# Kernel optimization log

Measured on AMD Instinct MI355X. Metric: run time of the kernel, lower is better.

## Reference

```python
import jax, jax.numpy as jnp
import numpy as np

B, T, D = 8, 128, 512


def setup_inputs() -> dict:
    key = jax.random.key(0)
    ks = jax.random.split(key, 13)
    s = 1.0 / np.sqrt(D)
    inp = {"x": jax.random.normal(ks[0], (B, T, D), dtype=jnp.float32)}
    names = ["qf", "kf", "vf", "qt", "kt", "vt"]
    for i, n in enumerate(names):
        inp[f"W_{n}"] = jax.random.uniform(ks[1 + 2 * i], (D, D), dtype=jnp.float32, minval=-s, maxval=s)
        inp[f"b_{n}"] = jax.random.uniform(ks[2 + 2 * i], (D,), dtype=jnp.float32, minval=-s, maxval=s)
    return inp


def reference(x, W_qf, b_qf, W_kf, b_kf, W_vf, b_vf, W_qt, b_qt, W_kt, b_kt, W_vt, b_vt):
    # torch nn.Linear stores weight as [out, in]: y = x @ W.T + b
    lin = lambda h, W, b: jnp.einsum('bti,oi->bto', h, W) + b

    # --- feature branch: elementwise Q*K scores, softmax over feature dim ---
    Q_f = lin(x, W_qf, b_qf)
    K_f = lin(x, W_kf, b_kf)
    V_f = lin(x, W_vf, b_vf)
    ctx_f = jax.nn.softmax(Q_f * K_f, axis=-1) * V_f  # [B,T,D]

    # --- temporal(-named) branch: per-(b,t) outer product over feature dim ---
    Q_t = lin(x, W_qt, b_qt)
    K_t = lin(x, W_kt, b_kt)
    V_t = lin(x, W_vt, b_vt)
    scores_t = jnp.einsum('bti,btj->btij', Q_t, K_t)          # [B,T,D,D]
    probs_t = jax.nn.softmax(scores_t, axis=-1)
    ctx_t = jnp.einsum('btij,btj->bti', probs_t, V_t)          # [B,T,D]

    # dropout is identity in eval mode
    return ctx_f + ctx_t
```

## Files before the change

### kernel.cpp

```cpp
#include <hip/hip_runtime.h>
#include <hip/hip_bf16.h>
#include <math.h>


#define M_ROWS 1024
#define DIMD   512
#define NCOLS  3072
#define KPHYS  1024

typedef __attribute__((ext_vector_type(8))) short short8;
typedef __attribute__((ext_vector_type(4))) float f32x4;

struct PtrArgs {
    const float* W[6];
    const float* b[6];
};

#define XN (M_ROWS * DIMD)
#define WN (NCOLS * DIMD)

__device__ __forceinline__ unsigned short bf16_rne(float v) {
    unsigned u = __float_as_uint(v);
    u = (u + 0x7FFFu + ((u >> 16) & 1u)) >> 16;
    return (unsigned short)u;
}

__device__ __constant__ float INVFACT[25] = {
    1.0f, 1.0f, 0.5f,
    1.6666666666666666e-01f, 4.1666666666666664e-02f, 8.3333333333333332e-03f,
    1.3888888888888889e-03f, 1.9841269841269841e-04f, 2.4801587301587302e-05f,
    2.7557319223985893e-06f, 2.7557319223985888e-07f, 2.5052108385441720e-08f,
    2.0876756987868100e-09f, 1.6059043836821613e-10f, 1.1470745597729725e-11f,
    7.6471637318198164e-13f, 4.7794773323873853e-14f, 2.8114572543455206e-15f,
    1.5619206968586225e-16f, 8.2206352466243295e-18f, 4.1103176233121648e-19f,
    1.9572941063391263e-20f, 8.8967913924505741e-22f, 3.8681701706306835e-23f,
    1.6117375710961184e-24f
};

__global__ __launch_bounds__(256) void convert_split(const float* __restrict__ x,
                                                     PtrArgs pa,
                                                     unsigned short* __restrict__ Aph,
                                                     unsigned short* __restrict__ Bph,
                                                     float* __restrict__ biasAll) {
    int idx = blockIdx.x * 256 + threadIdx.x;
    if (idx < NCOLS) {
        biasAll[idx] = pa.b[idx >> 9][idx & 511];
    }
    if (idx < XN) {
        int m = idx >> 9, k = idx & 511;
        int s = k >> 5, p = k & 31;
        float v = x[idx];
        unsigned short hb = bf16_rne(v);
        float hf = __uint_as_float(((unsigned)hb) << 16);
        unsigned short lb = bf16_rne(v - hf);
        Aph[(size_t)m * KPHYS + s * 64 + p]      = hb;
        Aph[(size_t)m * KPHYS + s * 64 + 32 + p] = lb;
    } else if (idx < XN + WN) {
        int j = idx - XN;
        int n = j >> 9, k = j & 511;
        int g = n >> 9, o = n & 511;
        int s = k >> 5, p = k & 31;
        float v = pa.W[g][(size_t)o * DIMD + k];
        unsigned short hb = bf16_rne(v);
        float hf = __uint_as_float(((unsigned)hb) << 16);
        unsigned short lb = bf16_rne(v - hf);
        Bph[(size_t)n * KPHYS + s * 64 + p]      = hb;
        Bph[(size_t)n * KPHYS + s * 64 + 32 + p] = lb;
    }
}

__global__ __launch_bounds__(256) void gemm_mfma(const unsigned short* __restrict__ A,
                                                 const unsigned short* __restrict__ B,
                                                 const float* __restrict__ biasAll,
                                                 float* __restrict__ Y) {
    __shared__ __align__(16) short As[64 * 128];
    __shared__ __align__(16) short Bs[128 * 128];

    const int tid  = threadIdx.x;
    const int m0   = blockIdx.y * 64;
    const int n0   = blockIdx.x * 128;
    const int lane = tid & 63;
    const int w    = tid >> 6;
    const int wm   = w & 1;
    const int wn   = w >> 1;
    const int l15  = lane & 15;
    const int quad = lane >> 4;

    f32x4 acc[2][4];
    #pragma unroll
    for (int i = 0; i < 2; ++i)
        #pragma unroll
        for (int j = 0; j < 4; ++j)
            acc[i][j] = (f32x4){0.f, 0.f, 0.f, 0.f};

    for (int it = 0; it < 8; ++it) {
        const int kbase = it * 128;
        __syncthreads();
        #pragma unroll
        for (int t = 0; t < 4; ++t) {
            int idx = t * 256 + tid;
            int r = idx >> 4, c = idx & 15;
            int cc = c ^ (r & 15);
            const unsigned short* ga = A + (size_t)(m0 + r) * KPHYS + kbase + cc * 8;
            __builtin_amdgcn_global_load_lds(
                (const __attribute__((address_space(1))) unsigned int*)ga,
                (__attribute__((address_space(3))) unsigned int*)&As[idx * 8], 16, 0, 0);
        }
        #pragma unroll
        for (int t = 0; t < 8; ++t) {
            int idx = t * 256 + tid;
            int r = idx >> 4, c = idx & 15;
            int cc = c ^ (r & 15);
            const unsigned short* gb = B + (size_t)(n0 + r) * KPHYS + kbase + cc * 8;
            __builtin_amdgcn_global_load_lds(
                (const __attribute__((address_space(1))) unsigned int*)gb,
                (__attribute__((address_space(3))) unsigned int*)&Bs[idx * 8], 16, 0, 0);
        }
        __syncthreads();

        #pragma unroll
        for (int kk = 0; kk < 2; ++kk) {
            short8 ah[2], al[2], bh[4], bl[4];
            #pragma unroll
            for (int mt = 0; mt < 2; ++mt) {
                int rA = wm * 32 + mt * 16 + l15;
                int ch = (kk * 8 + quad)     ^ (rA & 15);
                int cl = (kk * 8 + 4 + quad) ^ (rA & 15);
                ah[mt] = *(const short8*)&As[(rA * 16 + ch) * 8];
                al[mt] = *(const short8*)&As[(rA * 16 + cl) * 8];
            }
            #pragma unroll
            for (int nt = 0; nt < 4; ++nt) {
                int rB = wn * 64 + nt * 16 + l15;
                int ch = (kk * 8 + quad)     ^ (rB & 15);
                int cl = (kk * 8 + 4 + quad) ^ (rB & 15);
                bh[nt] = *(const short8*)&Bs[(rB * 16 + ch) * 8];
                bl[nt] = *(const short8*)&Bs[(rB * 16 + cl) * 8];
            }
            #pragma unroll
            for (int mt = 0; mt < 2; ++mt)
                #pragma unroll
                for (int nt = 0; nt < 4; ++nt) {
                    acc[mt][nt] = __builtin_amdgcn_mfma_f32_16x16x32_bf16(
                        ah[mt], bh[nt], acc[mt][nt], 0, 0, 0);
                    acc[mt][nt] = __builtin_amdgcn_mfma_f32_16x16x32_bf16(
                        ah[mt], bl[nt], acc[mt][nt], 0, 0, 0);
                    acc[mt][nt] = __builtin_amdgcn_mfma_f32_16x16x32_bf16(
                        al[mt], bh[nt], acc[mt][nt], 0, 0, 0);
                }
        }
    }

    #pragma unroll
    for (int nt = 0; nt < 4; ++nt) {
        int col = n0 + wn * 64 + nt * 16 + l15;
        float bv = biasAll[col];
        #pragma unroll
        for (int mt = 0; mt < 2; ++mt) {
            int row0 = m0 + wm * 32 + mt * 16 + quad * 4;
            #pragma unroll
            for (int r = 0; r < 4; ++r)
                Y[(size_t)(row0 + r) * NCOLS + col] = acc[mt][nt][r] + bv;
        }
    }
}

#define PSTR 53

__global__ __launch_bounds__(64) void fused_attn(const float* __restrict__ Y,
                                                 float* __restrict__ out) {
    const int row = blockIdx.x;
    const int l   = threadIdx.x;
    const float* __restrict__ Yr = Y + (size_t)row * NCOLS;
    const int i0 = l * 8;

    __shared__ float part[64 * PSTR];
    __shared__ float cbuf[50];

    const float LOG2E = 1.4426950408889634f;

    float4 qf0 = *(const float4*)(Yr + i0);
    float4 qf1 = *(const float4*)(Yr + i0 + 4);
    float4 kf0 = *(const float4*)(Yr + 512 + i0);
    float4 kf1 = *(const float4*)(Yr + 512 + i0 + 4);
    float4 vf0 = *(const float4*)(Yr + 1024 + i0);
    float4 vf1 = *(const float4*)(Yr + 1024 + i0 + 4);
    float4 qt0 = *(const float4*)(Yr + 1536 + i0);
    float4 qt1 = *(const float4*)(Yr + 1536 + i0 + 4);
    float4 kt0 = *(const float4*)(Yr + 2048 + i0);
    float4 kt1 = *(const float4*)(Yr + 2048 + i0 + 4);
    float4 vt0 = *(const float4*)(Yr + 2560 + i0);
    float4 vt1 = *(const float4*)(Yr + 2560 + i0 + 4);

    float e[8];
    e[0] = __builtin_amdgcn_exp2f(qf0.x * kf0.x * LOG2E);
    e[1] = __builtin_amdgcn_exp2f(qf0.y * kf0.y * LOG2E);
    e[2] = __builtin_amdgcn_exp2f(qf0.z * kf0.z * LOG2E);
    e[3] = __builtin_amdgcn_exp2f(qf0.w * kf0.w * LOG2E);
    e[4] = __builtin_amdgcn_exp2f(qf1.x * kf1.x * LOG2E);
    e[5] = __builtin_amdgcn_exp2f(qf1.y * kf1.y * LOG2E);
    e[6] = __builtin_amdgcn_exp2f(qf1.z * kf1.z * LOG2E);
    e[7] = __builtin_amdgcn_exp2f(qf1.w * kf1.w * LOG2E);
    float psum = ((e[0] + e[1]) + (e[2] + e[3])) + ((e[4] + e[5]) + (e[6] + e[7]));
    #pragma unroll
    for (int off = 32; off; off >>= 1) psum += __shfl_xor(psum, off);
    const float invS = 1.0f / psum;

    float k[8] = {kt0.x, kt0.y, kt0.z, kt0.w, kt1.x, kt1.y, kt1.z, kt1.w};
    float v[8] = {vt0.x, vt0.y, vt0.z, vt0.w, vt1.x, vt1.y, vt1.z, vt1.w};
    float kp[8] = {1.f, 1.f, 1.f, 1.f, 1.f, 1.f, 1.f, 1.f};
    float* myrow = &part[l * PSTR];
    #pragma unroll
    for (int p = 0; p < 25; ++p) {
        float n = ((kp[0] + kp[1]) + (kp[2] + kp[3])) +
                  ((kp[4] + kp[5]) + (kp[6] + kp[7]));
        float m = fmaf(kp[7], v[7], fmaf(kp[6], v[6],
                  fmaf(kp[5], v[5], fmaf(kp[4], v[4],
                  fmaf(kp[3], v[3], fmaf(kp[2], v[2],
                  fmaf(kp[1], v[1], kp[0] * v[0])))))));
        myrow[p]      = m;
        myrow[25 + p] = n;
        #pragma unroll
        for (int j = 0; j < 8; ++j) kp[j] *= k[j];
    }
    __syncthreads();

    if (l < 50) {
        float s = 0.f;
        #pragma unroll
        for (int i = 0; i < 64; ++i) s += part[i * PSTR + l];
        cbuf[l] = s * INVFACT[l < 25 ? l : l - 25];
    }
    __syncthreads();

    float q[8] = {qt0.x, qt0.y, qt0.z, qt0.w, qt1.x, qt1.y, qt1.z, qt1.w};
    float F[8], G[8];
    {
        float cf = cbuf[24], cg = cbuf[49];
        #pragma unroll
        for (int c = 0; c < 8; ++c) { F[c] = cf; G[c] = cg; }
    }
    #pragma unroll
    for (int p = 23; p >= 0; --p) {
        float cf = cbuf[p], cg = cbuf[25 + p];
        #pragma unroll
        for (int c = 0; c < 8; ++c) {
            F[c] = fmaf(F[c], q[c], cf);
            G[c] = fmaf(G[c], q[c], cg);
        }
    }

    float4 o0, o1;
    o0.x = e[0] * invS * vf0.x + F[0] / G[0];
    o0.y = e[1] * invS * vf0.y + F[1] / G[1];
    o0.z = e[2] * invS * vf0.z + F[2] / G[2];
    o0.w = e[3] * invS * vf0.w + F[3] / G[3];
    o1.x = e[4] * invS * vf1.x + F[4] / G[4];
    o1.y = e[5] * invS * vf1.y + F[5] / G[5];
    o1.z = e[6] * invS * vf1.z + F[6] / G[6];
    o1.w = e[7] * invS * vf1.w + F[7] / G[7];
    *(float4*)(out + (size_t)row * DIMD + i0)     = o0;
    *(float4*)(out + (size_t)row * DIMD + i0 + 4) = o1;
}

extern "C" void kernel_launch(void* const* d_in, const int* in_sizes, int n_in,
                              void* d_out, int out_size, void* d_ws, size_t ws_size,
                              hipStream_t stream) {
    const float* x = (const float*)d_in[0];
    PtrArgs pa;
    for (int g = 0; g < 6; ++g) {
        pa.W[g] = (const float*)d_in[1 + 2 * g];
        pa.b[g] = (const float*)d_in[2 + 2 * g];
    }

    char* ws = (char*)d_ws;
    float*          Y    = (float*)ws;
    unsigned short* Aph  = (unsigned short*)(ws + 12582912);
    unsigned short* Bph  = (unsigned short*)(ws + 12582912 + 2097152);
    float*          bias = (float*)(ws + 12582912 + 2097152 + 6291456);

    convert_split<<<(XN + WN) / 256, 256, 0, stream>>>(x, pa, Aph, Bph, bias);

    dim3 g1(NCOLS / 128, M_ROWS / 64);
    gemm_mfma<<<g1, 256, 0, stream>>>(Aph, Bph, bias, Y);

    fused_attn<<<M_ROWS, 64, 0, stream>>>(Y, (float*)d_out);
}
```

Before: 108.0 us.

## Double-buffer GEMM LDS tiles and vectorize the bf16 split conversion

```diff
diff --git a/kernel.cpp b/kernel.cpp
--- a/kernel.cpp
+++ b/kernel.cpp
@@ -10,6 +10,7 @@
 
 typedef __attribute__((ext_vector_type(8))) short short8;
 typedef __attribute__((ext_vector_type(4))) float f32x4;
+typedef __attribute__((ext_vector_type(4))) unsigned short u16x4;
 
 struct PtrArgs {
     const float* W[6];
@@ -42,30 +43,35 @@
                                                      unsigned short* __restrict__ Aph,
                                                      unsigned short* __restrict__ Bph,
                                                      float* __restrict__ biasAll) {
-    int idx = blockIdx.x * 256 + threadIdx.x;
+    const int idx = blockIdx.x * 256 + threadIdx.x;
     if (idx < NCOLS) {
         biasAll[idx] = pa.b[idx >> 9][idx & 511];
     }
-    if (idx < XN) {
-        int m = idx >> 9, k = idx & 511;
+    const int e4 = idx * 4;
+    if (e4 < XN) {
+        int m = e4 >> 9, k = e4 & 511;
         int s = k >> 5, p = k & 31;
-        float v = x[idx];
-        unsigned short hb = bf16_rne(v);
-        float hf = __uint_as_float(((unsigned)hb) << 16);
-        unsigned short lb = bf16_rne(v - hf);
-        Aph[(size_t)m * KPHYS + s * 64 + p]      = hb;
-        Aph[(size_t)m * KPHYS + s * 64 + 32 + p] = lb;
-    } else if (idx < XN + WN) {
-        int j = idx - XN;
+        float4 v = *(const float4*)(x + e4);
+        u16x4 hi, lo;
+        hi.x = bf16_rne(v.x); lo.x = bf16_rne(v.x - __uint_as_float(((unsigned)hi.x) << 16));
+        hi.y = bf16_rne(v.y); lo.y = bf16_rne(v.y - __uint_as_float(((unsigned)hi.y) << 16));
+        hi.z = bf16_rne(v.z); lo.z = bf16_rne(v.z - __uint_as_float(((unsigned)hi.z) << 16));
+        hi.w = bf16_rne(v.w); lo.w = bf16_rne(v.w - __uint_as_float(((unsigned)hi.w) << 16));
+        *(u16x4*)&Aph[(size_t)m * KPHYS + s * 64 + p]      = hi;
+        *(u16x4*)&Aph[(size_t)m * KPHYS + s * 64 + 32 + p] = lo;
+    } else if (e4 < XN + WN) {
+        int j = e4 - XN;
         int n = j >> 9, k = j & 511;
         int g = n >> 9, o = n & 511;
         int s = k >> 5, p = k & 31;
-        float v = pa.W[g][(size_t)o * DIMD + k];
-        unsigned short hb = bf16_rne(v);
-        float hf = __uint_as_float(((unsigned)hb) << 16);
-        unsigned short lb = bf16_rne(v - hf);
-        Bph[(size_t)n * KPHYS + s * 64 + p]      = hb;
-        Bph[(size_t)n * KPHYS + s * 64 + 32 + p] = lb;
+        float4 v = *(const float4*)(pa.W[g] + (size_t)o * DIMD + k);
+        u16x4 hi, lo;
+        hi.x = bf16_rne(v.x); lo.x = bf16_rne(v.x - __uint_as_float(((unsigned)hi.x) << 16));
+        hi.y = bf16_rne(v.y); lo.y = bf16_rne(v.y - __uint_as_float(((unsigned)hi.y) << 16));
+        hi.z = bf16_rne(v.z); lo.z = bf16_rne(v.z - __uint_as_float(((unsigned)hi.z) << 16));
+        hi.w = bf16_rne(v.w); lo.w = bf16_rne(v.w - __uint_as_float(((unsigned)hi.w) << 16));
+        *(u16x4*)&Bph[(size_t)n * KPHYS + s * 64 + p]      = hi;
+        *(u16x4*)&Bph[(size_t)n * KPHYS + s * 64 + 32 + p] = lo;
     }
 }
 
@@ -73,8 +79,8 @@
                                                  const unsigned short* __restrict__ B,
                                                  const float* __restrict__ biasAll,
                                                  float* __restrict__ Y) {
-    __shared__ __align__(16) short As[64 * 128];
-    __shared__ __align__(16) short Bs[128 * 128];
+    __shared__ __align__(16) short As[2][64 * 64];
+    __shared__ __align__(16) short Bs[2][128 * 64];
 
     const int tid  = threadIdx.x;
     const int m0   = blockIdx.y * 64;
@@ -93,62 +99,66 @@
         for (int j = 0; j < 4; ++j)
             acc[i][j] = (f32x4){0.f, 0.f, 0.f, 0.f};
 
-    for (int it = 0; it < 8; ++it) {
-        const int kbase = it * 128;
-        __syncthreads();
-        #pragma unroll
-        for (int t = 0; t < 4; ++t) {
+    auto stage = [&](int it, int buf) {
+        const int kbase = it * 64;
+        #pragma unroll
+        for (int t = 0; t < 2; ++t) {
             int idx = t * 256 + tid;
-            int r = idx >> 4, c = idx & 15;
-            int cc = c ^ (r & 15);
+            int r = idx >> 3, c = idx & 7;
+            int cc = c ^ (r & 7);
             const unsigned short* ga = A + (size_t)(m0 + r) * KPHYS + kbase + cc * 8;
             __builtin_amdgcn_global_load_lds(
                 (const __attribute__((address_space(1))) unsigned int*)ga,
-                (__attribute__((address_space(3))) unsigned int*)&As[idx * 8], 16, 0, 0);
-        }
-        #pragma unroll
-        for (int t = 0; t < 8; ++t) {
+                (__attribute__((address_space(3))) unsigned int*)&As[buf][idx * 8], 16, 0, 0);
+        }
+        #pragma unroll
+        for (int t = 0; t < 4; ++t) {
             int idx = t * 256 + tid;
-            int r = idx >> 4, c = idx & 15;
-            int cc = c ^ (r & 15);
+            int r = idx >> 3, c = idx & 7;
+            int cc = c ^ (r & 7);
             const unsigned short* gb = B + (size_t)(n0 + r) * KPHYS + kbase + cc * 8;
             __builtin_amdgcn_global_load_lds(
                 (const __attribute__((address_space(1))) unsigned int*)gb,
-                (__attribute__((address_space(3))) unsigned int*)&Bs[idx * 8], 16, 0, 0);
-        }
+                (__attribute__((address_space(3))) unsigned int*)&Bs[buf][idx * 8], 16, 0, 0);
+        }
+    };
+
+    stage(0, 0);
+
+    for (int it = 0; it < 16; ++it) {
         __syncthreads();
-
-        #pragma unroll
-        for (int kk = 0; kk < 2; ++kk) {
-            short8 ah[2], al[2], bh[4], bl[4];
-            #pragma unroll
-            for (int mt = 0; mt < 2; ++mt) {
-                int rA = wm * 32 + mt * 16 + l15;
-                int ch = (kk * 8 + quad)     ^ (rA & 15);
-                int cl = (kk * 8 + 4 + quad) ^ (rA & 15);
-                ah[mt] = *(const short8*)&As[(rA * 16 + ch) * 8];
-                al[mt] = *(const short8*)&As[(rA * 16 + cl) * 8];
-            }
+        if (it + 1 < 16) stage(it + 1, (it + 1) & 1);
+
+        const short* as = As[it & 1];
+        const short* bs = Bs[it & 1];
+        short8 ah[2], al[2], bh[4], bl[4];
+        #pragma unroll
+        for (int mt = 0; mt < 2; ++mt) {
+            int rA = wm * 32 + mt * 16 + l15;
+            int ch = quad ^ (rA & 7);
+            int cl = (4 + quad) ^ (rA & 7);
+            ah[mt] = *(const short8*)&as[(rA * 8 + ch) * 8];
+            al[mt] = *(const short8*)&as[(rA * 8 + cl) * 8];
+        }
+        #pragma unroll
+        for (int nt = 0; nt < 4; ++nt) {
+            int rB = wn * 64 + nt * 16 + l15;
+            int ch = quad ^ (rB & 7);
+            int cl = (4 + quad) ^ (rB & 7);
+            bh[nt] = *(const short8*)&bs[(rB * 8 + ch) * 8];
+            bl[nt] = *(const short8*)&bs[(rB * 8 + cl) * 8];
+        }
+        #pragma unroll
+        for (int mt = 0; mt < 2; ++mt)
             #pragma unroll
             for (int nt = 0; nt < 4; ++nt) {
-                int rB = wn * 64 + nt * 16 + l15;
-                int ch = (kk * 8 + quad)     ^ (rB & 15);
-                int cl = (kk * 8 + 4 + quad) ^ (rB & 15);
-                bh[nt] = *(const short8*)&Bs[(rB * 16 + ch) * 8];
-                bl[nt] = *(const short8*)&Bs[(rB * 16 + cl) * 8];
+                acc[mt][nt] = __builtin_amdgcn_mfma_f32_16x16x32_bf16(
+                    ah[mt], bh[nt], acc[mt][nt], 0, 0, 0);
+                acc[mt][nt] = __builtin_amdgcn_mfma_f32_16x16x32_bf16(
+                    ah[mt], bl[nt], acc[mt][nt], 0, 0, 0);
+                acc[mt][nt] = __builtin_amdgcn_mfma_f32_16x16x32_bf16(
+                    al[mt], bh[nt], acc[mt][nt], 0, 0, 0);
             }
-            #pragma unroll
-            for (int mt = 0; mt < 2; ++mt)
-                #pragma unroll
-                for (int nt = 0; nt < 4; ++nt) {
-                    acc[mt][nt] = __builtin_amdgcn_mfma_f32_16x16x32_bf16(
-                        ah[mt], bh[nt], acc[mt][nt], 0, 0, 0);
-                    acc[mt][nt] = __builtin_amdgcn_mfma_f32_16x16x32_bf16(
-                        ah[mt], bl[nt], acc[mt][nt], 0, 0, 0);
-                    acc[mt][nt] = __builtin_amdgcn_mfma_f32_16x16x32_bf16(
-                        al[mt], bh[nt], acc[mt][nt], 0, 0, 0);
-                }
-        }
     }
 
     #pragma unroll
@@ -279,7 +289,7 @@
     unsigned short* Bph  = (unsigned short*)(ws + 12582912 + 2097152);
     float*          bias = (float*)(ws + 12582912 + 2097152 + 6291456);
 
-    convert_split<<<(XN + WN) / 256, 256, 0, stream>>>(x, pa, Aph, Bph, bias);
+    convert_split<<<(XN + WN) / 4 / 256, 256, 0, stream>>>(x, pa, Aph, Bph, bias);
 
     dim3 g1(NCOLS / 128, M_ROWS / 64);
     gemm_mfma<<<g1, 256, 0, stream>>>(Aph, Bph, bias, Y);
```

Result: faster. 105.1 us (-2.6%).
